# Optimization experiments

Measured on AMD Instinct MI355X. Metric: run time of the kernel, lower is better.

The kernel has to match this reference:

```python
import jax, jax.numpy as jnp
import numpy as np

B, L, F, P = 128, 256, 4, 4   # dialogs, dialog length, future/past links
IN, H, C = 1024, 256, 7
N = B * L


def _build_edges():
    # same structure as build_intra_graph: self-loop + F future + P past per node
    i = np.arange(L)
    ss, tt = [], []
    for d in range(-P, F + 1):
        j = i + d
        m = (j >= 0) & (j < L)
        ss.append(i[m]); tt.append(j[m])
    s = np.concatenate(ss); t = np.concatenate(tt)
    offs = (np.arange(B) * L)[:, None]
    S = (s[None, :] + offs).ravel()
    T = (t[None, :] + offs).ravel()
    return np.stack([S, T]).astype(np.int32)


def setup_inputs() -> dict:
    key = jax.random.key(0)
    ks = jax.random.split(key, 16)
    ei = _build_edges()
    speakers = np.asarray(jax.random.randint(ks[0], (N,), 0, 2), dtype=np.int32)
    rel = (speakers[ei[0]] * speakers[ei[1]]).astype(np.int32)
    sd_in = 1.0 / np.sqrt(IN)
    sd_h = 1.0 / np.sqrt(H)
    return {
        "input": jax.random.normal(ks[1], (N, IN), jnp.float32),
        "dialog_lengths": jnp.full((B,), L, jnp.int32),
        "speakers": jnp.asarray(speakers),
        "labels": jax.random.randint(ks[2], (N,), 0, C, jnp.int32),
        "edge_index": jnp.asarray(ei),
        "rel_type": jnp.asarray(rel),
        # RGCNConv(IN, H, num_relations=2): per-relation weight, root weight, bias
        "W_rgcn": jax.random.normal(ks[3], (2, IN, H), jnp.float32) * sd_in,
        "W_root": jax.random.normal(ks[4], (IN, H), jnp.float32) * sd_in,
        "b_rgcn": jax.random.normal(ks[5], (H,), jnp.float32) * 0.01,
        # GraphConv(H, H): lin_rel (on aggregated neighbors, with bias), lin_root (no bias)
        "W_rel": jax.random.normal(ks[6], (H, H), jnp.float32) * sd_h,
        "b_rel": jax.random.normal(ks[7], (H,), jnp.float32) * 0.01,
        "W_grt": jax.random.normal(ks[8], (H, H), jnp.float32) * sd_h,
        # skip_con: Linear(IN, H)
        "W_skip": jax.random.normal(ks[9], (IN, H), jnp.float32) * sd_in,
        "b_skip": jax.random.normal(ks[10], (H,), jnp.float32) * 0.01,
        # classify: Linear(H, C)
        "W_cls": jax.random.normal(ks[11], (H, C), jnp.float32) * sd_h,
        "b_cls": jax.random.normal(ks[12], (C,), jnp.float32) * 0.01,
    }


def reference(input, dialog_lengths, speakers, labels, edge_index, rel_type,
              W_rgcn, W_root, b_rgcn, W_rel, b_rel, W_grt,
              W_skip, b_skip, W_cls, b_cls):
    n = input.shape[0]
    src, dst = edge_index[0], edge_index[1]
    seg = jax.ops.segment_sum

    # --- RGCNConv: out_i = x_i @ W_root + b + sum_r mean_{j in N_r(i)} x_j @ W_r
    t = jnp.einsum('ni,rio->rno', input, W_rgcn)      # [2, N, H]
    msg = t[rel_type, src]                            # [E, H] relation-specific messages
    h = input @ W_root + b_rgcn
    for r in range(2):
        m = (rel_type == r).astype(input.dtype)       # [E]
        s = seg(msg * m[:, None], dst, num_segments=n)
        cnt = seg(m, dst, num_segments=n)
        h = h + s / jnp.maximum(cnt, 1.0)[:, None]    # mean aggregation per relation

    # --- GraphConv (aggr='add'): out_i = W_rel @ sum_j h_j + b_rel + W_grt @ h_i
    neigh = seg(h[src], dst, num_segments=n)          # [N, H]
    h2 = neigh @ W_rel + b_rel + h @ W_grt

    # --- skip connection + classifier
    out = (h2 + input @ W_skip + b_skip) @ W_cls + b_cls  # [N, C]

    # --- cross entropy (mean)
    logp = jax.nn.log_softmax(out, axis=-1)
    loss = -jnp.mean(jnp.take_along_axis(logp, labels[:, None].astype(jnp.int32), axis=1))
    return out, loss
```

## Files before the change

kernel.cpp:

```cpp
#include <hip/hip_runtime.h>

#define NN 32768
#define INF 1024
#define HF 256

typedef __bf16 bf16x8 __attribute__((ext_vector_type(8)));
typedef float f32x4 __attribute__((ext_vector_type(4)));
typedef unsigned short u16x8 __attribute__((ext_vector_type(8)));

__device__ __forceinline__ float bf2f(unsigned short u) {
  union { unsigned int i; float f; } v; v.i = ((unsigned int)u) << 16; return v.f;
}
__device__ __forceinline__ unsigned short f2bf(float f) {
  union { float f; unsigned int i; } v; v.f = f;
  unsigned int x = v.i;
  return (unsigned short)((x + 0x7fffu + ((x >> 16) & 1u)) >> 16);
}

__device__ __forceinline__ void ld_lds16(const unsigned short* g, unsigned short* l) {
  __builtin_amdgcn_global_load_lds(
      (__attribute__((address_space(1))) const unsigned int*)g,
      (__attribute__((address_space(3))) unsigned int*)l, 16, 0, 0);
}

__global__ __launch_bounds__(256)
void diagcn_prep(const float* __restrict__ x, const float* __restrict__ Wrgcn,
                 const float* __restrict__ Wroot, const float* __restrict__ Wskip,
                 const float* __restrict__ Wgrt, const float* __restrict__ Wrel,
                 unsigned short* __restrict__ Xbf, unsigned short* __restrict__ WbigT,
                 unsigned short* __restrict__ WsmT, float* __restrict__ loss) {
  int bid = blockIdx.x;
  if (bid < 16384) {
    if (bid == 0 && threadIdx.x == 0) loss[0] = 0.f;
    int gid = bid * 256 + threadIdx.x;
    const float4* xv = (const float4*)x;
    float4 a = xv[2 * gid], b2 = xv[2 * gid + 1];
    u16x8 o;
    o[0] = f2bf(a.x); o[1] = f2bf(a.y); o[2] = f2bf(a.z); o[3] = f2bf(a.w);
    o[4] = f2bf(b2.x); o[5] = f2bf(b2.y); o[6] = f2bf(b2.z); o[7] = f2bf(b2.w);
    *(u16x8*)&Xbf[(size_t)gid * 8] = o;
    return;
  }
  __shared__ float tile[64 * 65];
  int tb = bid - 16384;
  const float* src;
  int k0, ncol0;
  unsigned short* dst;
  int ldd, nrow0;
  if (tb < 256) {
    int tn = tb >> 4, tk = tb & 15;
    int mat = tn >> 2;
    src = (mat == 0) ? Wrgcn : (mat == 1) ? (Wrgcn + 262144) : (mat == 2) ? Wroot : Wskip;
    k0 = tk * 64; ncol0 = (tn & 3) * 64;
    dst = WbigT; ldd = 1024; nrow0 = tn * 64;
  } else {
    int t2 = tb - 256;
    int tn = t2 >> 3, tk = t2 & 7;
    src = (tk < 4) ? Wgrt : Wrel;
    k0 = (tk & 3) * 64; ncol0 = tn * 64;
    dst = WsmT; ldd = 512; nrow0 = tn * 64;
  }
  int kdst0 = (tb < 256) ? k0 : (((tb - 256) & 7) * 64);
  int c = threadIdx.x & 63, rb = threadIdx.x >> 6;
#pragma unroll
  for (int it = 0; it < 16; ++it) {
    int r = rb + it * 4;
    tile[r * 65 + c] = src[(size_t)(k0 + r) * 256 + ncol0 + c];
  }
  __syncthreads();
  int kk = threadIdx.x & 63;
#pragma unroll
  for (int it = 0; it < 16; ++it) {
    int nn = rb + it * 4;
    dst[(size_t)(nrow0 + nn) * ldd + kdst0 + kk] = f2bf(tile[kk * 65 + nn]);
  }
}

template<bool STG, int VM, bool LAST>
__device__ __forceinline__ void g1_tile(int t,
    const unsigned short* __restrict__ gA0, const unsigned short* __restrict__ gB0,
    unsigned short* SH, int w, int abase, int bbase, int sw8,
    bf16x8 (&av)[4], bf16x8 (&bv)[4], bf16x8 (&nav)[4], bf16x8 (&nbv)[4],
    f32x4 (&acc)[8][4]) {
  unsigned short* Ab = SH + ((t & 3) << 14);
  unsigned short* Bb = Ab + 8192;
  bf16x8 av2[4];
#pragma unroll
  for (int i = 0; i < 4; ++i)
    av2[i] = *(const bf16x8*)&Ab[(abase + 64 + i * 16) * 32 + sw8];
  __builtin_amdgcn_sched_barrier(0);
  if (STG) {
    unsigned short* dA = SH + (((t + 3) & 3) << 14) + (w << 10);
    const unsigned short* gA = gA0 + (t + 3) * 32;
    ld_lds16(gA, dA);
    ld_lds16(gA + 16 * 1024, dA + 512);
    unsigned short* dB = SH + (((t + 3) & 3) << 14) + 8192 + (w << 10);
    const unsigned short* gB = gB0 + (t + 3) * 32;
    ld_lds16(gB, dB);
    ld_lds16(gB + 16 * 1024, dB + 512);
  }
  asm volatile("s_waitcnt lgkmcnt(4)");
  __builtin_amdgcn_sched_barrier(0);
  __builtin_amdgcn_s_setprio(1);
#pragma unroll
  for (int i = 0; i < 4; ++i)
#pragma unroll
    for (int j = 0; j < 4; ++j)
      acc[i][j] = __builtin_amdgcn_mfma_f32_16x16x32_bf16(av[i], bv[j], acc[i][j], 0, 0, 0);
  __builtin_amdgcn_s_setprio(0);
  __builtin_amdgcn_sched_barrier(0);
  if constexpr (VM == 8) asm volatile("s_waitcnt vmcnt(8)" ::: "memory");
  else if constexpr (VM == 4) asm volatile("s_waitcnt vmcnt(4)" ::: "memory");
  else if constexpr (VM == 0) asm volatile("s_waitcnt vmcnt(0)" ::: "memory");
  __builtin_amdgcn_s_barrier();
  if constexpr (!LAST) {
    unsigned short* An = SH + (((t + 1) & 3) << 14);
    unsigned short* Bn = An + 8192;
#pragma unroll
    for (int i = 0; i < 4; ++i)
      nav[i] = *(const bf16x8*)&An[(abase + i * 16) * 32 + sw8];
    __builtin_amdgcn_sched_barrier(0);
    asm volatile("s_waitcnt lgkmcnt(4)");
    __builtin_amdgcn_sched_barrier(0);
    __builtin_amdgcn_s_setprio(1);
#pragma unroll
    for (int i = 0; i < 2; ++i)
#pragma unroll
      for (int j = 0; j < 4; ++j)
        acc[4 + i][j] = __builtin_amdgcn_mfma_f32_16x16x32_bf16(av2[i], bv[j], acc[4 + i][j], 0, 0, 0);
    __builtin_amdgcn_s_setprio(0);
    __builtin_amdgcn_sched_barrier(0);
#pragma unroll
    for (int j = 0; j < 4; ++j)
      nbv[j] = *(const bf16x8*)&Bn[(bbase + j * 16) * 32 + sw8];
    __builtin_amdgcn_sched_barrier(0);
    __builtin_amdgcn_s_setprio(1);
#pragma unroll
    for (int i = 2; i < 4; ++i)
#pragma unroll
      for (int j = 0; j < 4; ++j)
        acc[4 + i][j] = __builtin_amdgcn_mfma_f32_16x16x32_bf16(av2[i], bv[j], acc[4 + i][j], 0, 0, 0);
    __builtin_amdgcn_s_setprio(0);
    __builtin_amdgcn_s_barrier();
  } else {
    asm volatile("s_waitcnt lgkmcnt(0)");
    __builtin_amdgcn_sched_barrier(0);
#pragma unroll
    for (int i = 0; i < 4; ++i)
#pragma unroll
      for (int j = 0; j < 4; ++j)
        acc[4 + i][j] = __builtin_amdgcn_mfma_f32_16x16x32_bf16(av2[i], bv[j], acc[4 + i][j], 0, 0, 0);
  }
}

__global__ __launch_bounds__(512, 2)
void diagcn_gemm1(const unsigned short* __restrict__ A, const unsigned short* __restrict__ BT,
                  unsigned short* __restrict__ Y) {
  __shared__ unsigned short SH[65536];
  const int tid = threadIdx.x;
  const int w = tid >> 6, lane = tid & 63;
  const int quad = lane >> 4, l15 = lane & 15;
  const int wm = w >> 2, wn = w & 3;
  const int b = blockIdx.x;
  const int wg = ((b & 7) << 6) + (b >> 3);
  const int m0 = (wg >> 2) << 8;
  const int n0 = (wg & 3) << 8;
  const int abase = wm * 128 + l15;
  const int bbase = wn * 64 + l15;
  const int sw8 = ((quad ^ ((l15 >> 1) & 3)) << 3);
  const int csrc8 = (((lane & 3) ^ ((lane >> 3) & 3)) << 3);
  const unsigned short* gA0 = A + (size_t)(m0 + w * 32 + (lane >> 2)) * 1024 + csrc8;
  const unsigned short* gB0 = BT + (size_t)(n0 + w * 32 + (lane >> 2)) * 1024 + csrc8;

  f32x4 acc[8][4] = {};
  bf16x8 avA[4], bvA[4], avB[4], bvB[4];

#pragma unroll
  for (int tt = 0; tt < 3; ++tt) {
    unsigned short* dA = SH + (tt << 14) + (w << 10);
    ld_lds16(gA0 + tt * 32, dA);
    ld_lds16(gA0 + tt * 32 + 16 * 1024, dA + 512);
    unsigned short* dB = SH + (tt << 14) + 8192 + (w << 10);
    ld_lds16(gB0 + tt * 32, dB);
    ld_lds16(gB0 + tt * 32 + 16 * 1024, dB + 512);
  }
  asm volatile("s_waitcnt vmcnt(8)" ::: "memory");
  __builtin_amdgcn_s_barrier();
#pragma unroll
  for (int i = 0; i < 4; ++i)
    avA[i] = *(const bf16x8*)&SH[(abase + i * 16) * 32 + sw8];
#pragma unroll
  for (int j = 0; j < 4; ++j)
    bvA[j] = *(const bf16x8*)&SH[8192 + (bbase + j * 16) * 32 + sw8];
  __builtin_amdgcn_sched_barrier(0);

#pragma unroll 1
  for (int tt = 0; tt < 14; ++tt) {
    g1_tile<true, 8, false>(2 * tt, gA0, gB0, SH, w, abase, bbase, sw8,
                            avA, bvA, avB, bvB, acc);
    g1_tile<true, 8, false>(2 * tt + 1, gA0, gB0, SH, w, abase, bbase, sw8,
                            avB, bvB, avA, bvA, acc);
  }
  g1_tile<true, 8, false>(28, gA0, gB0, SH, w, abase, bbase, sw8, avA, bvA, avB, bvB, acc);
  g1_tile<false, 4, false>(29, gA0, gB0, SH, w, abase, bbase, sw8, avB, bvB, avA, bvA, acc);
  g1_tile<false, 0, false>(30, gA0, gB0, SH, w, abase, bbase, sw8, avA, bvA, avB, bvB, acc);
  g1_tile<false, -1, true>(31, gA0, gB0, SH, w, abase, bbase, sw8, avB, bvB, avA, bvA, acc);

#pragma unroll
  for (int i = 0; i < 8; ++i)
#pragma unroll
    for (int j = 0; j < 4; ++j) {
      const int row = m0 + wm * 128 + i * 16 + quad * 4;
      const int col = n0 + wn * 64 + j * 16 + l15;
#pragma unroll
      for (int r = 0; r < 4; ++r)
        Y[(size_t)(row + r) * 1024 + col] = f2bf(acc[i][j][r]);
    }
}

__global__ __launch_bounds__(256)
void diagcn_h(const unsigned short* __restrict__ Y, const int* __restrict__ spk,
              const float* __restrict__ brgcn, unsigned short* __restrict__ A2) {
  int b = blockIdx.x;
  int wv = threadIdx.x >> 6, lane = threadIdx.x & 63;
  int half = lane >> 5, li = lane & 31, c0 = li << 3;
  int node = ((b & 7) << 12) + ((b >> 3) << 3) + wv * 2 + half;
  int p = node & 255, dbase = node - p;
  int si = spk[node];
  float a0[8] = {}, a1[8] = {};
  float n0 = 0.f, n1 = 0.f;
#pragma unroll
  for (int d = -4; d <= 4; ++d) {
    int pj = p + d;
    float w = (pj >= 0 && pj < 256) ? 1.f : 0.f;
    int jc = pj < 0 ? 0 : (pj > 255 ? 255 : pj);
    int nj = dbase + jc;
    int rel = si & spk[nj];
    u16x8 v = *(const u16x8*)&Y[(size_t)nj * 1024 + (rel << 8) + c0];
    float w1 = rel ? w : 0.f, w0 = rel ? 0.f : w;
#pragma unroll
    for (int k = 0; k < 8; ++k) {
      float f = bf2f(v[k]);
      a0[k] += f * w0; a1[k] += f * w1;
    }
    n0 += w0; n1 += w1;
  }
  u16x8 vr = *(const u16x8*)&Y[(size_t)node * 1024 + 512 + c0];
  float i0 = 1.f / fmaxf(n0, 1.f), i1 = 1.f / fmaxf(n1, 1.f);
  u16x8 u;
#pragma unroll
  for (int k = 0; k < 8; ++k)
    u[k] = f2bf(bf2f(vr[k]) + brgcn[c0 + k] + a0[k] * i0 + a1[k] * i1);
  *(u16x8*)&A2[(size_t)node * 512 + c0] = u;
}

__global__ __launch_bounds__(256)
void diagcn_neigh(unsigned short* __restrict__ A2) {
  int b = blockIdx.x;
  int wv = threadIdx.x >> 6, lane = threadIdx.x & 63;
  int half = lane >> 5, li = lane & 31, c0 = li << 3;
  int node = ((b & 7) << 12) + ((b >> 3) << 3) + wv * 2 + half;
  int p = node & 255, dbase = node - p;
  float s[8] = {};
#pragma unroll
  for (int d = -4; d <= 4; ++d) {
    int pj = p + d;
    float w = (pj >= 0 && pj < 256) ? 1.f : 0.f;
    int jc = pj < 0 ? 0 : (pj > 255 ? 255 : pj);
    u16x8 v = *(const u16x8*)&A2[(size_t)(dbase + jc) * 512 + c0];
#pragma unroll
    for (int k = 0; k < 8; ++k) s[k] += bf2f(v[k]) * w;
  }
  u16x8 u;
#pragma unroll
  for (int k = 0; k < 8; ++k) u[k] = f2bf(s[k]);
  *(u16x8*)&A2[(size_t)node * 512 + 256 + c0] = u;
}

__global__ __launch_bounds__(256)
void diagcn_gemm2(const unsigned short* __restrict__ A, const unsigned short* __restrict__ BT,
                  const unsigned short* __restrict__ Y, const float* __restrict__ Wcls,
                  const float* __restrict__ bcls, const float* __restrict__ brel,
                  const float* __restrict__ bskip, const int* __restrict__ labels,
                  float* __restrict__ out, float* __restrict__ loss) {
  const int K = 512;
  __shared__ float Wc[2312];
  for (int i = threadIdx.x; i < 2312; i += 256) {
    float v;
    if (i < 1792) v = Wcls[i];
    else if (i < 1799) v = bcls[i - 1792];
    else if (i < 1800) v = 0.f;
    else if (i < 2056) v = brel[i - 1800];
    else v = bskip[i - 2056];
    Wc[i] = v;
  }
  __syncthreads();
  const int tid = threadIdx.x;
  const int w = tid >> 6, lane = tid & 63;
  const int quad = lane >> 4, l15 = lane & 15;
  const int b = blockIdx.x;
  const int m0 = (((b & 7) << 6) + (b >> 3)) << 6;

  f32x4 acc[16] = {};
  const unsigned short* Ab = A + (size_t)(m0 + w * 16 + l15) * K + quad * 8;
  const unsigned short* Bb = BT + (size_t)l15 * K + quad * 8;

#pragma unroll 2
  for (int k0 = 0; k0 < K; k0 += 64) {
#pragma unroll
    for (int ks = 0; ks < 2; ++ks) {
      bf16x8 av = *(const bf16x8*)(Ab + k0 + ks * 32);
#pragma unroll
      for (int j = 0; j < 16; ++j) {
        bf16x8 bv = *(const bf16x8*)(Bb + (size_t)j * 16 * K + k0 + ks * 32);
        acc[j] = __builtin_amdgcn_mfma_f32_16x16x32_bf16(av, bv, acc[j], 0, 0, 0);
      }
    }
  }

  float wsum[4][7] = {};
#pragma unroll
  for (int j = 0; j < 16; ++j) {
    int col = j * 16 + l15;
    float bb = Wc[1800 + col] + Wc[2056 + col];
#pragma unroll
    for (int r = 0; r < 4; ++r) {
      int row = m0 + w * 16 + quad * 4 + r;
      float z = acc[j][r] + bb + bf2f(Y[(size_t)row * 1024 + 768 + col]);
#pragma unroll
      for (int c = 0; c < 7; ++c) wsum[r][c] += z * Wc[col * 7 + c];
    }
  }
#pragma unroll
  for (int o = 1; o < 16; o <<= 1)
#pragma unroll
    for (int r = 0; r < 4; ++r)
#pragma unroll
      for (int c = 0; c < 7; ++c) wsum[r][c] += __shfl_xor(wsum[r][c], o, 64);

  float lsum = 0.f;
#pragma unroll
  for (int r = 0; r < 4; ++r) {
    int row = m0 + w * 16 + quad * 4 + r;
    float o7[7], mx = -1e30f;
#pragma unroll
    for (int c = 0; c < 7; ++c) {
      o7[c] = wsum[r][c] + Wc[1792 + c];
      mx = fmaxf(mx, o7[c]);
    }
    if (l15 < 7) out[(size_t)row * 7 + l15] = o7[l15];
    float s = 0.f;
#pragma unroll
    for (int c = 0; c < 7; ++c) s += expf(o7[c] - mx);
    int lab = labels[row];
    lsum += mx + logf(s) - o7[lab];
  }
  lsum += __shfl_xor(lsum, 16, 64);
  lsum += __shfl_xor(lsum, 32, 64);
  if (lane == 0) atomicAdd(loss, lsum * (1.0f / (float)NN));
}

extern "C" void kernel_launch(void* const* d_in, const int* in_sizes, int n_in,
                              void* d_out, int out_size, void* d_ws, size_t ws_size,
                              hipStream_t stream) {
  const float* x      = (const float*)d_in[0];
  const int* speakers = (const int*)d_in[2];
  const int* labels   = (const int*)d_in[3];
  const float* Wrgcn  = (const float*)d_in[6];
  const float* Wroot  = (const float*)d_in[7];
  const float* brgcn  = (const float*)d_in[8];
  const float* Wrel   = (const float*)d_in[9];
  const float* brel   = (const float*)d_in[10];
  const float* Wgrt   = (const float*)d_in[11];
  const float* Wskip  = (const float*)d_in[12];
  const float* bskip  = (const float*)d_in[13];
  const float* Wcls   = (const float*)d_in[14];
  const float* bcls   = (const float*)d_in[15];
  float* out = (float*)d_out;
  float* loss = out + (size_t)NN * 7;

  const size_t OFF_XBF  = 0;
  const size_t OFF_WBIG = 67108864;
  const size_t OFF_WSM  = 69206016;
  const size_t OFF_Y    = 69468160;
  const size_t OFF_A2   = 136577024;
  const size_t NEED     = 170131456;
  if (ws_size < NEED) return;

  char* ws = (char*)d_ws;
  unsigned short* Xbf   = (unsigned short*)(ws + OFF_XBF);
  unsigned short* WbigT = (unsigned short*)(ws + OFF_WBIG);
  unsigned short* WsmT  = (unsigned short*)(ws + OFF_WSM);
  unsigned short* Y     = (unsigned short*)(ws + OFF_Y);
  unsigned short* A2    = (unsigned short*)(ws + OFF_A2);

  diagcn_prep<<<dim3(16672), dim3(256), 0, stream>>>(x, Wrgcn, Wroot, Wskip, Wgrt, Wrel,
                                                     Xbf, WbigT, WsmT, loss);
  diagcn_gemm1<<<dim3(512), dim3(512), 0, stream>>>(Xbf, WbigT, Y);
  diagcn_h<<<dim3(NN / 8), dim3(256), 0, stream>>>(Y, speakers, brgcn, A2);
  diagcn_neigh<<<dim3(NN / 8), dim3(256), 0, stream>>>(A2);
  diagcn_gemm2<<<dim3(512), dim3(256), 0, stream>>>(A2, WsmT, Y, Wcls, bcls, brel, bskip,
                                                    labels, out, loss);
}
```

Baseline: 410.5 us.

## Stage gemm2 operands through swizzled LDS with double-buffered async loads

The second GEMM kernel used to read A and B fragments straight from global memory for each MFMA. It now copies 64-wide K tiles of A and B into XOR-swizzled shared memory with global_load_lds, double-buffered so the next tile loads while the current one is computed. The epilogue's Y slice is also staged through LDS, and the small classifier weights are read from global memory instead of a preloaded LDS table. This uses about 80KB of LDS per block, which may cut occupancy, and the manual waitcnt and barrier sequence has to be exactly right.

Result: faster. 371.0 us (-9.6%).

```diff
diff --git a/kernel.cpp b/kernel.cpp
--- a/kernel.cpp
+++ b/kernel.cpp
@@ -284,51 +284,93 @@
                   const float* __restrict__ bskip, const int* __restrict__ labels,
                   float* __restrict__ out, float* __restrict__ loss) {
   const int K = 512;
-  __shared__ float Wc[2312];
-  for (int i = threadIdx.x; i < 2312; i += 256) {
-    float v;
-    if (i < 1792) v = Wcls[i];
-    else if (i < 1799) v = bcls[i - 1792];
-    else if (i < 1800) v = 0.f;
-    else if (i < 2056) v = brel[i - 1800];
-    else v = bskip[i - 2056];
-    Wc[i] = v;
-  }
-  __syncthreads();
+  __shared__ unsigned short SH[40960];
   const int tid = threadIdx.x;
   const int w = tid >> 6, lane = tid & 63;
   const int quad = lane >> 4, l15 = lane & 15;
   const int b = blockIdx.x;
   const int m0 = (((b & 7) << 6) + (b >> 3)) << 6;
+  const int rowg = lane >> 3;
+  const int kbsw = (lane & 7) ^ rowg;
 
   f32x4 acc[16] = {};
-  const unsigned short* Ab = A + (size_t)(m0 + w * 16 + l15) * K + quad * 8;
-  const unsigned short* Bb = BT + (size_t)l15 * K + quad * 8;
-
-#pragma unroll 2
-  for (int k0 = 0; k0 < K; k0 += 64) {
-#pragma unroll
-    for (int ks = 0; ks < 2; ++ks) {
-      bf16x8 av = *(const bf16x8*)(Ab + k0 + ks * 32);
-#pragma unroll
-      for (int j = 0; j < 16; ++j) {
-        bf16x8 bv = *(const bf16x8*)(Bb + (size_t)j * 16 * K + k0 + ks * 32);
-        acc[j] = __builtin_amdgcn_mfma_f32_16x16x32_bf16(av, bv, acc[j], 0, 0, 0);
-      }
-    }
-  }
+  const unsigned short* Abase = A + (size_t)m0 * K + kbsw * 8;
+  const unsigned short* Bbase = BT + kbsw * 8;
+  const unsigned short* Ybase = Y + (size_t)(m0 + (lane >> 5)) * 1024 + 768 + (lane & 31) * 8;
+
+#define G2_STAGE(t, buf)                                                        \
+  {                                                                             \
+    unsigned short* As_ = SH + (buf) * 20480;                                   \
+    unsigned short* Bs_ = As_ + 4096;                                           \
+    int k0_ = (t) * 64;                                                         \
+    _Pragma("unroll")                                                           \
+    for (int i = 0; i < 2; ++i) {                                               \
+      int grp = w * 2 + i;                                                      \
+      ld_lds16(Abase + (size_t)(grp * 8 + rowg) * K + k0_, &As_[grp * 512]);    \
+    }                                                                           \
+    _Pragma("unroll")                                                           \
+    for (int i = 0; i < 8; ++i) {                                               \
+      int grp = w * 8 + i;                                                      \
+      ld_lds16(Bbase + (size_t)(grp * 8 + rowg) * K + k0_, &Bs_[grp * 512]);    \
+    }                                                                           \
+  }
+#define G2_COMPUTE(buf)                                                         \
+  {                                                                             \
+    const unsigned short* As_ = SH + (buf) * 20480;                             \
+    const unsigned short* Bs_ = As_ + 4096;                                     \
+    _Pragma("unroll")                                                           \
+    for (int ks = 0; ks < 2; ++ks) {                                            \
+      int kb = ks * 4 + quad;                                                   \
+      int ra = w * 16 + l15;                                                    \
+      bf16x8 av = *(const bf16x8*)&As_[ra * 64 + ((kb ^ (ra & 7)) << 3)];       \
+      _Pragma("unroll")                                                         \
+      for (int j = 0; j < 16; ++j) {                                            \
+        int rb2 = j * 16 + l15;                                                 \
+        bf16x8 bv = *(const bf16x8*)&Bs_[rb2 * 64 + ((kb ^ (rb2 & 7)) << 3)];   \
+        acc[j] = __builtin_amdgcn_mfma_f32_16x16x32_bf16(av, bv, acc[j], 0, 0, 0); \
+      }                                                                         \
+    }                                                                           \
+  }
+
+  G2_STAGE(0, 0);
+  G2_STAGE(1, 1);
+  asm volatile("s_waitcnt vmcnt(10)" ::: "memory");
+  __builtin_amdgcn_s_barrier();
+
+#pragma unroll 1
+  for (int t = 0; t < 6; ++t) {
+    G2_COMPUTE(t & 1);
+    asm volatile("s_waitcnt lgkmcnt(0)" ::: "memory");
+    __builtin_amdgcn_s_barrier();
+    G2_STAGE(t + 2, t & 1);
+    asm volatile("s_waitcnt vmcnt(10)" ::: "memory");
+    __builtin_amdgcn_s_barrier();
+  }
+  G2_COMPUTE(0);
+  asm volatile("s_waitcnt lgkmcnt(0)" ::: "memory");
+  __builtin_amdgcn_s_barrier();
+  asm volatile("s_waitcnt vmcnt(0)" ::: "memory");
+  __builtin_amdgcn_s_barrier();
+#pragma unroll
+  for (int i = 0; i < 8; ++i) {
+    int g = w * 8 + i;
+    ld_lds16(Ybase + (size_t)g * 2048, &SH[g * 512]);
+  }
+  G2_COMPUTE(1);
+  asm volatile("s_waitcnt vmcnt(0)" ::: "memory");
+  __builtin_amdgcn_s_barrier();
 
   float wsum[4][7] = {};
 #pragma unroll
   for (int j = 0; j < 16; ++j) {
     int col = j * 16 + l15;
-    float bb = Wc[1800 + col] + Wc[2056 + col];
+    float bb = brel[col] + bskip[col];
 #pragma unroll
     for (int r = 0; r < 4; ++r) {
-      int row = m0 + w * 16 + quad * 4 + r;
-      float z = acc[j][r] + bb + bf2f(Y[(size_t)row * 1024 + 768 + col]);
-#pragma unroll
-      for (int c = 0; c < 7; ++c) wsum[r][c] += z * Wc[col * 7 + c];
+      int rl = w * 16 + quad * 4 + r;
+      float z = acc[j][r] + bb + bf2f(SH[rl * 256 + col]);
+#pragma unroll
+      for (int c = 0; c < 7; ++c) wsum[r][c] += z * Wcls[col * 7 + c];
     }
   }
 #pragma unroll
@@ -345,7 +387,7 @@
     float o7[7], mx = -1e30f;
 #pragma unroll
     for (int c = 0; c < 7; ++c) {
-      o7[c] = wsum[r][c] + Wc[1792 + c];
+      o7[c] = wsum[r][c] + bcls[c];
       mx = fmaxf(mx, o7[c]);
     }
     if (l15 < 7) out[(size_t)row * 7 + l15] = o7[l15];
@@ -358,6 +400,8 @@
   lsum += __shfl_xor(lsum, 16, 64);
   lsum += __shfl_xor(lsum, 32, 64);
   if (lane == 0) atomicAdd(loss, lsum * (1.0f / (float)NN));
+#undef G2_STAGE
+#undef G2_COMPUTE
 }
 
 extern "C" void kernel_launch(void* const* d_in, const int* in_sizes, int n_in,
```
